# Optimization experiments

Hardware: AMD Instinct MI355X
Metric: run time of the kernel (lower is better)

Reference implementation:

```python
import jax, jax.numpy as jnp
import numpy as np

INPUT_DIM = 1024
HIDDEN_DIM = 1024
NUM_HEADS = 16
HEAD_DIM = HIDDEN_DIM // NUM_HEADS


def setup_inputs() -> dict:
    key = jax.random.key(0)
    ks = jax.random.split(key, 11)
    B, S = 2, 2048
    s_in = 1.0 / np.sqrt(INPUT_DIM)
    s_hid = 1.0 / np.sqrt(HIDDEN_DIM)
    return {
        "query": jax.random.normal(ks[0], (B, S, INPUT_DIM), jnp.float32),
        "key": jax.random.normal(ks[1], (B, S, INPUT_DIM), jnp.float32),
        "value": jax.random.normal(ks[2], (B, S, INPUT_DIM), jnp.float32),
        "Wq": jax.random.normal(ks[3], (INPUT_DIM, HIDDEN_DIM), jnp.float32) * s_in,
        "bq": jnp.zeros((HIDDEN_DIM,), jnp.float32),
        "Wk": jax.random.normal(ks[4], (INPUT_DIM, HEAD_DIM), jnp.float32) * s_in,
        "bk": jnp.zeros((HEAD_DIM,), jnp.float32),
        "Wv": jax.random.normal(ks[5], (INPUT_DIM, HEAD_DIM), jnp.float32) * s_in,
        "bv": jnp.zeros((HEAD_DIM,), jnp.float32),
        "Wo": jax.random.normal(ks[6], (HIDDEN_DIM, INPUT_DIM), jnp.float32) * s_hid,
        "bo": jnp.zeros((INPUT_DIM,), jnp.float32),
    }


def reference(query, key, value, Wq, bq, Wk, bk, Wv, bv, Wo, bo):
    B, S, _ = query.shape
    # projections
    q = query @ Wq + bq                       # [B,S,H*D]
    k = key @ Wk + bk                         # [B,S,D]  (single shared head)
    v = value @ Wv + bv                       # [B,S,D]
    q = q.reshape(B, S, NUM_HEADS, HEAD_DIM)  # [B,S,H,D]
    # MQA scores: shared K broadcast over query heads
    scores = jnp.einsum('bqhd,bkd->bhqk', q, k) / np.sqrt(HIDDEN_DIM)
    attn = jax.nn.softmax(scores, axis=-1)    # [B,H,Q,K]
    out = jnp.einsum('bhqk,bkd->bqhd', attn, v)  # [B,Q,H,D]
    out = out.reshape(B, S, HIDDEN_DIM)
    return out @ Wo + bo
```

## Files before the change

kernel.cpp:

```cpp
#include <hip/hip_runtime.h>


typedef unsigned int   u32;
typedef unsigned short u16;
typedef union { float4 v; float f[4]; } f4u;
typedef __attribute__((ext_vector_type(8)))  short frag16;
typedef __attribute__((ext_vector_type(4)))  float f32x4;
typedef __attribute__((ext_vector_type(16))) float f32x16;
typedef union { frag16 v; u32 w[4]; u16 e[8]; } bf8u;

static __device__ __forceinline__ u16 f2bf(float x) {
  union { float f; u32 u; } v; v.f = x;
  u32 r = v.u + 0x7fff + ((v.u >> 16) & 1);
  return (u16)(r >> 16);
}

static __device__ __forceinline__ u32 cvt_pk_bf16(float lo, float hi) {
  u32 r;
  asm("v_cvt_pk_bf16_f32 %0, %1, %2" : "=v"(r) : "v"(lo), "v"(hi));
  return r;
}

static __device__ __forceinline__ void gload_lds16(const u16* g, u16* l) {
  __builtin_amdgcn_global_load_lds(
      (const __attribute__((address_space(1))) u32*)g,
      (__attribute__((address_space(3))) u32*)l, 16, 0, 0);
}

static __device__ void tcvt_tile(const float* __restrict__ src,
                                 u16* __restrict__ dst,
                                 int C, int ldT, int rt, int ct,
                                 float (*t)[65]) {
  const int r0 = rt * 64, c0 = ct * 64;
  const int tr  = threadIdx.x >> 4;
  const int tc4 = (threadIdx.x & 15) * 4;
#pragma unroll
  for (int i = 0; i < 4; ++i) {
    f4u v; v.v = *(const float4*)(src + (size_t)(r0 + tr + i * 16) * C + c0 + tc4);
    t[tr + i * 16][tc4 + 0] = v.f[0];
    t[tr + i * 16][tc4 + 1] = v.f[1];
    t[tr + i * 16][tc4 + 2] = v.f[2];
    t[tr + i * 16][tc4 + 3] = v.f[3];
  }
  __syncthreads();
#pragma unroll
  for (int i = 0; i < 4; ++i) {
    const int oc = tr + i * 16;
    ushort4 o;
    o.x = f2bf(t[tc4 + 0][oc]);
    o.y = f2bf(t[tc4 + 1][oc]);
    o.z = f2bf(t[tc4 + 2][oc]);
    o.w = f2bf(t[tc4 + 3][oc]);
    *(ushort4*)(dst + (size_t)(c0 + oc) * ldT + r0 + tc4) = o;
  }
}

__global__ __launch_bounds__(256)
void prep_w(const float* __restrict__ Wq, const float* __restrict__ Wo,
            const float* __restrict__ Wk, const float* __restrict__ Wv,
            const float* __restrict__ query,
            u16* __restrict__ wq_t, u16* __restrict__ wo_t,
            u16* __restrict__ wk_t, u16* __restrict__ wv_t,
            u16* __restrict__ xq_bf) {
  const int bid = blockIdx.x;
  if (bid >= 544) {
    const size_t base = (size_t)(bid - 544) * 4096 + threadIdx.x * 16;
    f4u x0, x1, x2, x3;
    x0.v = *(const float4*)(query + base);
    x1.v = *(const float4*)(query + base + 4);
    x2.v = *(const float4*)(query + base + 8);
    x3.v = *(const float4*)(query + base + 12);
    bf8u t0, t1;
    t0.w[0] = cvt_pk_bf16(x0.f[0], x0.f[1]);
    t0.w[1] = cvt_pk_bf16(x0.f[2], x0.f[3]);
    t0.w[2] = cvt_pk_bf16(x1.f[0], x1.f[1]);
    t0.w[3] = cvt_pk_bf16(x1.f[2], x1.f[3]);
    t1.w[0] = cvt_pk_bf16(x2.f[0], x2.f[1]);
    t1.w[1] = cvt_pk_bf16(x2.f[2], x2.f[3]);
    t1.w[2] = cvt_pk_bf16(x3.f[0], x3.f[1]);
    t1.w[3] = cvt_pk_bf16(x3.f[2], x3.f[3]);
    *(frag16*)(xq_bf + base)     = t0.v;
    *(frag16*)(xq_bf + base + 8) = t1.v;
    return;
  }
  __shared__ float t[64][65];
  if (bid < 256)      tcvt_tile(Wq, wq_t, 1024, 1024, bid >> 4, bid & 15, t);
  else if (bid < 512) tcvt_tile(Wo, wo_t, 1024, 1024, (bid - 256) >> 4, (bid - 256) & 15, t);
  else if (bid < 528) tcvt_tile(Wk, wk_t, 64, 1024, bid - 512, 0, t);
  else                tcvt_tile(Wv, wv_t, 64, 1024, bid - 528, 0, t);
}

static __device__ void gemm128n64(const u16* __restrict__ Abf,
                                  const u16* __restrict__ Bt,
                                  const float* __restrict__ bias,
                                  void* __restrict__ Cout, int out_mode,
                                  float oscale, int row0, int col0,
                                  int N, int K, u16* As, u16* Bs) {
  const int tid  = threadIdx.x;
  const int lane = tid & 63;
  const int quad = lane >> 4, l15 = lane & 15;
  const int w = tid >> 6, wy = w >> 1, wx = w & 1;
  const int lrow = lane >> 3, lcol = (lane & 7) * 8;

  f32x4 acc[4][2];
#pragma unroll
  for (int i = 0; i < 4; ++i)
#pragma unroll
    for (int j = 0; j < 2; ++j) {
      acc[i][j][0] = 0.f; acc[i][j][1] = 0.f;
      acc[i][j][2] = 0.f; acc[i][j][3] = 0.f;
    }

  const u16* ag = Abf + (size_t)(row0 + w * 32 + lrow) * K + lcol;
  const u16* bg = Bt  + (size_t)(col0 + w * 16 + lrow) * K + lcol;
  u16* alds = As + w * 4 * 512;
  u16* blds = Bs + w * 2 * 512;

  for (int k0 = 0; k0 < K; k0 += 64) {
    __syncthreads();
#pragma unroll
    for (int i = 0; i < 4; ++i)
      gload_lds16(ag + (size_t)i * 8 * K + k0, alds + i * 512);
#pragma unroll
    for (int i = 0; i < 2; ++i)
      gload_lds16(bg + (size_t)i * 8 * K + k0, blds + i * 512);
    __syncthreads();
#pragma unroll
    for (int ks = 0; ks < 2; ++ks) {
      frag16 af[4], bfr[2];
#pragma unroll
      for (int i = 0; i < 4; ++i)
        af[i] = *(const frag16*)(&As[(wy * 64 + i * 16 + l15) * 64 + ks * 32 + quad * 8]);
#pragma unroll
      for (int j = 0; j < 2; ++j)
        bfr[j] = *(const frag16*)(&Bs[(wx * 32 + j * 16 + l15) * 64 + ks * 32 + quad * 8]);
#pragma unroll
      for (int i = 0; i < 4; ++i)
#pragma unroll
        for (int j = 0; j < 2; ++j)
          acc[i][j] = __builtin_amdgcn_mfma_f32_16x16x32_bf16(af[i], bfr[j], acc[i][j], 0, 0, 0);
    }
  }

  float bj[2];
#pragma unroll
  for (int j = 0; j < 2; ++j)
    bj[j] = bias[col0 + wx * 32 + j * 16 + l15];

#pragma unroll
  for (int i = 0; i < 4; ++i)
#pragma unroll
    for (int rr = 0; rr < 4; ++rr) {
      const size_t row = row0 + wy * 64 + i * 16 + quad * 4 + rr;
#pragma unroll
      for (int j = 0; j < 2; ++j) {
        const float v = (acc[i][j][rr] + bj[j]) * oscale;
        const int col = col0 + wx * 32 + j * 16 + l15;
        if (out_mode == 0) ((float*)Cout)[row * N + col] = v;
        else               ((u16*)Cout)[row * N + col] = f2bf(v);
      }
    }
}

#define GP 72
template <bool A_FP32>
static __device__ void gemm64(const float* __restrict__ Af32,
                              const u16* __restrict__ Abf,
                              const u16* __restrict__ Bt,
                              const float* __restrict__ bias,
                              void* __restrict__ Cout, int out_mode,
                              float oscale,
                              int row0, int col0, int N, int K, int ldT,
                              u16* As, u16* Bs) {
  const int tid  = threadIdx.x;
  const int lane = tid & 63;
  const int quad = lane >> 4, l15 = lane & 15;
  const int w = tid >> 6, wy = w >> 1, wx = w & 1;

  f32x4 acc[2][2];
#pragma unroll
  for (int i = 0; i < 2; ++i)
#pragma unroll
    for (int j = 0; j < 2; ++j) {
      acc[i][j][0] = 0.f; acc[i][j][1] = 0.f;
      acc[i][j][2] = 0.f; acc[i][j][3] = 0.f;
    }

  const int r = tid >> 2, c16 = (tid & 3) * 16;

  for (int k0 = 0; k0 < K; k0 += 64) {
    frag16 a0, a1;
    if (A_FP32) {
      const float* ap = Af32 + (size_t)(row0 + r) * K + k0 + c16;
      f4u x0, x1, x2, x3;
      x0.v = *(const float4*)(ap);
      x1.v = *(const float4*)(ap + 4);
      x2.v = *(const float4*)(ap + 8);
      x3.v = *(const float4*)(ap + 12);
      bf8u t0, t1;
      t0.w[0] = cvt_pk_bf16(x0.f[0], x0.f[1]);
      t0.w[1] = cvt_pk_bf16(x0.f[2], x0.f[3]);
      t0.w[2] = cvt_pk_bf16(x1.f[0], x1.f[1]);
      t0.w[3] = cvt_pk_bf16(x1.f[2], x1.f[3]);
      t1.w[0] = cvt_pk_bf16(x2.f[0], x2.f[1]);
      t1.w[1] = cvt_pk_bf16(x2.f[2], x2.f[3]);
      t1.w[2] = cvt_pk_bf16(x3.f[0], x3.f[1]);
      t1.w[3] = cvt_pk_bf16(x3.f[2], x3.f[3]);
      a0 = t0.v; a1 = t1.v;
    } else {
      const u16* ap = Abf + (size_t)(row0 + r) * K + k0 + c16;
      a0 = *(const frag16*)(ap);
      a1 = *(const frag16*)(ap + 8);
    }
    const u16* bp = Bt + (size_t)(col0 + r) * K + k0 + c16;
    const frag16 b0 = *(const frag16*)(bp);
    const frag16 b1 = *(const frag16*)(bp + 8);
    __syncthreads();
    *(frag16*)(&As[r * GP + c16])     = a0;
    *(frag16*)(&As[r * GP + c16 + 8]) = a1;
    *(frag16*)(&Bs[r * GP + c16])     = b0;
    *(frag16*)(&Bs[r * GP + c16 + 8]) = b1;
    __syncthreads();
#pragma unroll
    for (int ks = 0; ks < 2; ++ks) {
      frag16 af[2], bf[2];
#pragma unroll
      for (int i = 0; i < 2; ++i)
        af[i] = *(const frag16*)(&As[(wy * 32 + i * 16 + l15) * GP + ks * 32 + quad * 8]);
#pragma unroll
      for (int j = 0; j < 2; ++j)
        bf[j] = *(const frag16*)(&Bs[(wx * 32 + j * 16 + l15) * GP + ks * 32 + quad * 8]);
#pragma unroll
      for (int i = 0; i < 2; ++i)
#pragma unroll
        for (int j = 0; j < 2; ++j)
          acc[i][j] = __builtin_amdgcn_mfma_f32_16x16x32_bf16(af[i], bf[j], acc[i][j], 0, 0, 0);
    }
  }

  float bj[2];
#pragma unroll
  for (int j = 0; j < 2; ++j)
    bj[j] = bias[col0 + wx * 32 + j * 16 + l15];

#pragma unroll
  for (int i = 0; i < 2; ++i) {
#pragma unroll
    for (int rr = 0; rr < 4; ++rr) {
      const size_t row = row0 + wy * 32 + i * 16 + quad * 4 + rr;
#pragma unroll
      for (int j = 0; j < 2; ++j) {
        const float v = (acc[i][j][rr] + bj[j]) * oscale;
        const int col = col0 + wx * 32 + j * 16 + l15;
        if (out_mode == 0)      ((float*)Cout)[row * N + col] = v;
        else if (out_mode == 1) ((u16*)Cout)[row * N + col] = f2bf(v);
        else                    ((u16*)Cout)[(size_t)col * ldT + row] = f2bf(v);
      }
    }
  }
}

#define C2_SCALE 0.045084220027780106f

__global__ __launch_bounds__(256, 4)
void proj2(const float* __restrict__ key, const float* __restrict__ value,
           const u16* __restrict__ xq_bf,
           const u16* __restrict__ wq_t, const u16* __restrict__ wk_t,
           const u16* __restrict__ wv_t,
           const float* __restrict__ bq, const float* __restrict__ bk,
           const float* __restrict__ bv,
           u16* __restrict__ q_bf, u16* __restrict__ k_bf,
           u16* __restrict__ vt_bf, int M, int K) {
  __shared__ __align__(16) u16 smem[12288];
  const int bid = blockIdx.x;
  if (bid < 512)
    gemm128n64(xq_bf, wq_t, bq, q_bf, 1, C2_SCALE,
               (bid >> 4) * 128, (bid & 15) * 64, 1024, K, smem, smem + 8192);
  else if (bid < 576)
    gemm64<true>(key, nullptr, wk_t, bk, k_bf, 1, 1.0f,
                 (bid - 512) * 64, 0, 64, K, 0, smem, smem + 64 * GP);
  else
    gemm64<true>(value, nullptr, wv_t, bv, vt_bf, 2, 1.0f,
                 (bid - 576) * 64, 0, 64, K, M, smem, smem + 64 * GP);
}

__global__ __launch_bounds__(256, 4)
void out_proj(const u16* __restrict__ ao, const u16* __restrict__ wo_t,
              const float* __restrict__ bo, float* __restrict__ out,
              int M, int K) {
  __shared__ __align__(16) u16 smem[12288];
  const int bid = blockIdx.x;
  gemm128n64(ao, wo_t, bo, out, 0, 1.0f,
             (bid >> 4) * 128, (bid & 15) * 64, 1024, K, smem, smem + 8192);
}

#define PP 72

__global__ __launch_bounds__(256, 2)
void mqa_flash_mfma(const u16* __restrict__ Qb,
                    const u16* __restrict__ Kb,
                    const u16* __restrict__ Vt,
                    u16* __restrict__ O) {
  const int S = 2048, HID = 1024, D = 64, BS = 4096;
  __shared__ __align__(16) u16 Kss[64 * PP];
  __shared__ __align__(16) u16 Vss[64 * PP];
  __shared__ __align__(16) u16 Ps[4][32 * PP];
  __shared__ float lred[4][32];

  const int tid  = threadIdx.x;
  const int lane = tid & 63;
  const int w    = tid >> 6;
  const int l31  = lane & 31;
  const int hh   = lane >> 5;
  const int qb = blockIdx.x, hg = blockIdx.y, b = blockIdx.z;
  const int h = hg * 4 + w;

  const int sr = tid >> 3;
  const int sc = (tid & 7) * 8;

  const u16* kfb0 = &Kss[l31 * PP + hh * 8];
  const u16* kfb1 = &Kss[(32 + l31) * PP + hh * 8];
  const u16* vfb0 = &Vss[l31 * PP + hh * 8];
  const u16* vfb1 = &Vss[(32 + l31) * PP + hh * 8];
  u16* kw0 = &Kss[sr * PP + sc];
  u16* kw1 = &Kss[(sr + 32) * PP + sc];
  u16* vw0 = &Vss[sr * PP + sc];
  u16* vw1 = &Vss[(sr + 32) * PP + sc];
  u16* psw = Ps[w];
  u16* prow = &psw[l31 * PP];
  const u16* prd = &psw[l31 * PP + hh * 8];

  const u16* qrow = Qb + (size_t)(b * S + qb * 32 + l31) * HID + h * D;
  frag16 qf[4];
#pragma unroll
  for (int ks = 0; ks < 4; ++ks)
    qf[ks] = *(const frag16*)(qrow + ks * 16 + hh * 8);

  f32x16 zero16;
#pragma unroll
  for (int r = 0; r < 16; ++r) zero16[r] = 0.f;
  f32x16 oa0, oa1;
#pragma unroll
  for (int r = 0; r < 16; ++r) { oa0[r] = 0.f; oa1[r] = 0.f; }
  float l_lane = 0.f;

  const u16* kbase = Kb + (size_t)(b * S) * D;
  const u16* vbase = Vt + (size_t)(b * S);

  frag16 pk0 = *(const frag16*)(kbase + (size_t)sr * D + sc);
  frag16 pk1 = *(const frag16*)(kbase + (size_t)(sr + 32) * D + sc);
  frag16 pv0 = *(const frag16*)(vbase + (size_t)sr * BS + sc);
  frag16 pv1 = *(const frag16*)(vbase + (size_t)(sr + 32) * BS + sc);
  *(frag16*)kw0 = pk0;
  *(frag16*)kw1 = pk1;
  *(frag16*)vw0 = pv0;
  *(frag16*)vw1 = pv1;
  pk0 = *(const frag16*)(kbase + (size_t)(64 + sr) * D + sc);
  pk1 = *(const frag16*)(kbase + (size_t)(64 + sr + 32) * D + sc);
  pv0 = *(const frag16*)(vbase + (size_t)sr * BS + 64 + sc);
  pv1 = *(const frag16*)(vbase + (size_t)(sr + 32) * BS + 64 + sc);
  __syncthreads();

  for (int kc = 0; kc < S; kc += 64) {
    frag16 kf0[4], kf1[4], vf0[4], vf1[4];
#pragma unroll
    for (int ks = 0; ks < 4; ++ks) {
      kf0[ks] = *(const frag16*)(kfb0 + ks * 16);
      kf1[ks] = *(const frag16*)(kfb1 + ks * 16);
      vf0[ks] = *(const frag16*)(vfb0 + ks * 16);
      vf1[ks] = *(const frag16*)(vfb1 + ks * 16);
    }
    __syncthreads();

    *(frag16*)kw0 = pk0;
    *(frag16*)kw1 = pk1;
    *(frag16*)vw0 = pv0;
    *(frag16*)vw1 = pv1;

    const int nc = (kc + 128 < S) ? kc + 128 : (S - 64);
    pk0 = *(const frag16*)(kbase + (size_t)(nc + sr) * D + sc);
    pk1 = *(const frag16*)(kbase + (size_t)(nc + sr + 32) * D + sc);
    pv0 = *(const frag16*)(vbase + (size_t)sr * BS + nc + sc);
    pv1 = *(const frag16*)(vbase + (size_t)(sr + 32) * BS + nc + sc);

    f32x16 sa0, sa1;
#pragma unroll
    for (int ks = 0; ks < 4; ++ks)
      sa0 = __builtin_amdgcn_mfma_f32_32x32x16_bf16(kf0[ks], qf[ks], ks ? sa0 : zero16, 0, 0, 0);
#pragma unroll
    for (int ks = 0; ks < 4; ++ks)
      sa1 = __builtin_amdgcn_mfma_f32_32x32x16_bf16(kf1[ks], qf[ks], ks ? sa1 : zero16, 0, 0, 0);

#pragma unroll
    for (int g = 0; g < 4; ++g) {
      const float p0 = __builtin_amdgcn_exp2f(sa0[g * 4 + 0]);
      const float p1 = __builtin_amdgcn_exp2f(sa0[g * 4 + 1]);
      const float p2 = __builtin_amdgcn_exp2f(sa0[g * 4 + 2]);
      const float p3 = __builtin_amdgcn_exp2f(sa0[g * 4 + 3]);
      const float q0 = __builtin_amdgcn_exp2f(sa1[g * 4 + 0]);
      const float q1 = __builtin_amdgcn_exp2f(sa1[g * 4 + 1]);
      const float q2 = __builtin_amdgcn_exp2f(sa1[g * 4 + 2]);
      const float q3 = __builtin_amdgcn_exp2f(sa1[g * 4 + 3]);
      l_lane += ((p0 + p1) + (p2 + p3)) + ((q0 + q1) + (q2 + q3));
      uint2 pk;
      pk.x = cvt_pk_bf16(p0, p1); pk.y = cvt_pk_bf16(p2, p3);
      *(uint2*)(&prow[g * 8 + hh * 4]) = pk;
      uint2 qk;
      qk.x = cvt_pk_bf16(q0, q1); qk.y = cvt_pk_bf16(q2, q3);
      *(uint2*)(&prow[32 + g * 8 + hh * 4]) = qk;
    }

#pragma unroll
    for (int ks = 0; ks < 4; ++ks) {
      const frag16 pf = *(const frag16*)(prd + ks * 16);
      oa0 = __builtin_amdgcn_mfma_f32_32x32x16_bf16(pf, vf0[ks], oa0, 0, 0, 0);
      oa1 = __builtin_amdgcn_mfma_f32_32x32x16_bf16(pf, vf1[ks], oa1, 0, 0, 0);
    }

    __syncthreads();
  }

  l_lane += __shfl_xor(l_lane, 32);
  lred[w][l31] = l_lane;

#pragma unroll
  for (int g2 = 0; g2 < 4; ++g2) {
    const f32x4 lv = *(const f32x4*)(&lred[w][g2 * 8 + hh * 4]);
#pragma unroll
    for (int m = 0; m < 4; ++m) {
      const int r = g2 * 4 + m;
      const int q_local = g2 * 8 + hh * 4 + m;
      const float li = 1.f / lv[m];
      u16* orow = O + (size_t)(b * S + qb * 32 + q_local) * HID + h * D;
      orow[l31]      = f2bf(oa0[r] * li);
      orow[32 + l31] = f2bf(oa1[r] * li);
    }
  }
}

extern "C" void kernel_launch(void* const* d_in, const int* in_sizes, int n_in,
                              void* d_out, int out_size, void* d_ws, size_t ws_size,
                              hipStream_t stream) {
  const float* query = (const float*)d_in[0];
  const float* key   = (const float*)d_in[1];
  const float* value = (const float*)d_in[2];
  const float* Wq    = (const float*)d_in[3];
  const float* bq    = (const float*)d_in[4];
  const float* Wk    = (const float*)d_in[5];
  const float* bk    = (const float*)d_in[6];
  const float* Wv    = (const float*)d_in[7];
  const float* bv    = (const float*)d_in[8];
  const float* Wo    = (const float*)d_in[9];
  const float* bo    = (const float*)d_in[10];
  float* out = (float*)d_out;

  const int B = 2, S = 2048, IN = 1024, HID = 1024, H = 16, D = 64;
  const int M = B * S;
  const size_t MB = 1024 * 1024;

  char* ws = (char*)d_ws;
  u16* q_bf  = (u16*)ws;
  u16* ao_bf = (u16*)(ws + 8 * MB);
  u16* xq_bf = ao_bf;
  u16* k_bf  = (u16*)(ws + 16 * MB);
  u16* vt_bf = (u16*)(ws + 16 * MB + 512 * 1024);
  u16* wq_t  = (u16*)(ws + 17 * MB);
  u16* wo_t  = (u16*)(ws + 19 * MB);
  u16* wk_t  = (u16*)(ws + 21 * MB);
  u16* wv_t  = (u16*)(ws + 21 * MB + 128 * 1024);

  dim3 blk(256);
  prep_w<<<dim3(1568), blk, 0, stream>>>(Wq, Wo, Wk, Wv, query,
                                         wq_t, wo_t, wk_t, wv_t, xq_bf);
  proj2<<<dim3(640), blk, 0, stream>>>(key, value, xq_bf, wq_t, wk_t, wv_t,
                                       bq, bk, bv, q_bf, k_bf, vt_bf, M, IN);
  mqa_flash_mfma<<<dim3(S / 32, H / 4, B), blk, 0, stream>>>(q_bf, k_bf, vt_bf, ao_bf);
  out_proj<<<dim3(512), blk, 0, stream>>>(ao_bf, wo_t, bo, out, M, HID);
}
```

Before: 204.0 us.

## Split MQA attention over two key halves with a separate combine kernel

Splits the flash-attention key loop into two halves processed by separate blocks, writing unnormalized fp32 partial outputs and row sums to workspace. A new combine kernel then adds the partials, normalizes and converts to bf16. The goal is to double the block count for better occupancy across CUs. In exchange it adds an extra launch and substantial fp32 partial traffic (two 16MB buffers), and it only runs when the workspace is large enough. Because the softmax has no max subtraction, the two halves can simply be added.

```diff
diff --git a/kernel.cpp b/kernel.cpp
--- a/kernel.cpp
+++ b/kernel.cpp
@@ -295,26 +295,20 @@
 }
 
 #define PP 72
-
-__global__ __launch_bounds__(256, 2)
-void mqa_flash_mfma(const u16* __restrict__ Qb,
-                    const u16* __restrict__ Kb,
-                    const u16* __restrict__ Vt,
-                    u16* __restrict__ O) {
+#define SPLIT_ROWS 4096
+
+template <int NCHUNK>
+static __device__ void mqa_body(const u16* __restrict__ Qb,
+                                const u16* __restrict__ kbase,
+                                const u16* __restrict__ vbase,
+                                int qb, int h, int b,
+                                f32x16& oa0, f32x16& oa1, float& l_lane,
+                                u16* Kss, u16* Vss, u16* psw) {
   const int S = 2048, HID = 1024, D = 64, BS = 4096;
-  __shared__ __align__(16) u16 Kss[64 * PP];
-  __shared__ __align__(16) u16 Vss[64 * PP];
-  __shared__ __align__(16) u16 Ps[4][32 * PP];
-  __shared__ float lred[4][32];
-
   const int tid  = threadIdx.x;
   const int lane = tid & 63;
-  const int w    = tid >> 6;
   const int l31  = lane & 31;
   const int hh   = lane >> 5;
-  const int qb = blockIdx.x, hg = blockIdx.y, b = blockIdx.z;
-  const int h = hg * 4 + w;
-
   const int sr = tid >> 3;
   const int sc = (tid & 7) * 8;
 
@@ -326,7 +320,6 @@
   u16* kw1 = &Kss[(sr + 32) * PP + sc];
   u16* vw0 = &Vss[sr * PP + sc];
   u16* vw1 = &Vss[(sr + 32) * PP + sc];
-  u16* psw = Ps[w];
   u16* prow = &psw[l31 * PP];
   const u16* prd = &psw[l31 * PP + hh * 8];
 
@@ -339,13 +332,8 @@
   f32x16 zero16;
 #pragma unroll
   for (int r = 0; r < 16; ++r) zero16[r] = 0.f;
-  f32x16 oa0, oa1;
-#pragma unroll
-  for (int r = 0; r < 16; ++r) { oa0[r] = 0.f; oa1[r] = 0.f; }
-  float l_lane = 0.f;
-
-  const u16* kbase = Kb + (size_t)(b * S) * D;
-  const u16* vbase = Vt + (size_t)(b * S);
+
+  const int KEYS = NCHUNK * 64;
 
   frag16 pk0 = *(const frag16*)(kbase + (size_t)sr * D + sc);
   frag16 pk1 = *(const frag16*)(kbase + (size_t)(sr + 32) * D + sc);
@@ -361,7 +349,7 @@
   pv1 = *(const frag16*)(vbase + (size_t)(sr + 32) * BS + 64 + sc);
   __syncthreads();
 
-  for (int kc = 0; kc < S; kc += 64) {
+  for (int kc = 0; kc < KEYS; kc += 64) {
     frag16 kf0[4], kf1[4], vf0[4], vf1[4];
 #pragma unroll
     for (int ks = 0; ks < 4; ++ks) {
@@ -377,7 +365,7 @@
     *(frag16*)vw0 = pv0;
     *(frag16*)vw1 = pv1;
 
-    const int nc = (kc + 128 < S) ? kc + 128 : (S - 64);
+    const int nc = (kc + 128 < KEYS) ? kc + 128 : (KEYS - 64);
     pk0 = *(const frag16*)(kbase + (size_t)(nc + sr) * D + sc);
     pk1 = *(const frag16*)(kbase + (size_t)(nc + sr + 32) * D + sc);
     pv0 = *(const frag16*)(vbase + (size_t)sr * BS + nc + sc);
@@ -419,6 +407,104 @@
 
     __syncthreads();
   }
+}
+
+__global__ __launch_bounds__(256, 4)
+void mqa_flash_split(const u16* __restrict__ Qb, const u16* __restrict__ Kb,
+                     const u16* __restrict__ Vt,
+                     float* __restrict__ Opart,
+                     float* __restrict__ Lpart) {
+  const int S = 2048, HID = 1024, D = 64;
+  __shared__ __align__(16) u16 Kss[64 * PP];
+  __shared__ __align__(16) u16 Vss[64 * PP];
+  __shared__ __align__(16) u16 Ps[4][32 * PP];
+  __shared__ float lred[4][32];
+
+  const int tid  = threadIdx.x;
+  const int lane = tid & 63;
+  const int w    = tid >> 6;
+  const int l31  = lane & 31;
+  const int hh   = lane >> 5;
+  const int qb = blockIdx.x, hg = blockIdx.y;
+  const int b  = blockIdx.z >> 1, h2 = blockIdx.z & 1;
+  const int h = hg * 4 + w;
+
+  f32x16 oa0, oa1;
+#pragma unroll
+  for (int r = 0; r < 16; ++r) { oa0[r] = 0.f; oa1[r] = 0.f; }
+  float l_lane = 0.f;
+
+  const u16* kbase = Kb + (size_t)(b * S + h2 * 1024) * D;
+  const u16* vbase = Vt + (size_t)(b * S) + h2 * 1024;
+
+  mqa_body<16>(Qb, kbase, vbase, qb, h, b, oa0, oa1, l_lane, Kss, Vss, Ps[w]);
+
+  l_lane += __shfl_xor(l_lane, 32);
+  const int brow = b * S + qb * 32;
+  if (lane < 32)
+    Lpart[((size_t)h2 * SPLIT_ROWS + brow + l31) * 16 + h] = l_lane;
+
+  float* obase = Opart + (size_t)h2 * SPLIT_ROWS * 1024;
+#pragma unroll
+  for (int g2 = 0; g2 < 4; ++g2) {
+#pragma unroll
+    for (int m = 0; m < 4; ++m) {
+      const int r = g2 * 4 + m;
+      const int q_local = g2 * 8 + hh * 4 + m;
+      float* orow = obase + (size_t)(brow + q_local) * HID + h * D;
+      orow[l31]      = oa0[r];
+      orow[32 + l31] = oa1[r];
+    }
+  }
+}
+
+__global__ __launch_bounds__(256)
+void mqa_combine(const float* __restrict__ Opart, const float* __restrict__ Lpart,
+                 u16* __restrict__ ao) {
+  const int row = blockIdx.x;
+  const int tid = threadIdx.x;
+  const size_t base = (size_t)row * 1024 + tid * 4;
+  f4u a, c;
+  a.v = *(const float4*)(Opart + base);
+  c.v = *(const float4*)(Opart + (size_t)SPLIT_ROWS * 1024 + base);
+  const int hidx = tid >> 4;
+  const float l0 = Lpart[(size_t)row * 16 + hidx];
+  const float l1 = Lpart[((size_t)SPLIT_ROWS + row) * 16 + hidx];
+  const float li = 1.f / (l0 + l1);
+  ushort4 o;
+  o.x = f2bf((a.f[0] + c.f[0]) * li);
+  o.y = f2bf((a.f[1] + c.f[1]) * li);
+  o.z = f2bf((a.f[2] + c.f[2]) * li);
+  o.w = f2bf((a.f[3] + c.f[3]) * li);
+  *(ushort4*)(ao + base) = o;
+}
+
+__global__ __launch_bounds__(256, 2)
+void mqa_flash_mfma(const u16* __restrict__ Qb, const u16* __restrict__ Kb,
+                    const u16* __restrict__ Vt, u16* __restrict__ O) {
+  const int S = 2048, HID = 1024, D = 64;
+  __shared__ __align__(16) u16 Kss[64 * PP];
+  __shared__ __align__(16) u16 Vss[64 * PP];
+  __shared__ __align__(16) u16 Ps[4][32 * PP];
+  __shared__ float lred[4][32];
+
+  const int tid  = threadIdx.x;
+  const int lane = tid & 63;
+  const int w    = tid >> 6;
+  const int l31  = lane & 31;
+  const int hh   = lane >> 5;
+  const int qb = blockIdx.x, hg = blockIdx.y, b = blockIdx.z;
+  const int h = hg * 4 + w;
+
+  f32x16 oa0, oa1;
+#pragma unroll
+  for (int r = 0; r < 16; ++r) { oa0[r] = 0.f; oa1[r] = 0.f; }
+  float l_lane = 0.f;
+
+  const u16* kbase = Kb + (size_t)(b * S) * D;
+  const u16* vbase = Vt + (size_t)(b * S);
+
+  mqa_body<32>(Qb, kbase, vbase, qb, h, b, oa0, oa1, l_lane, Kss, Vss, Ps[w]);
 
   l_lane += __shfl_xor(l_lane, 32);
   lred[w][l31] = l_lane;
@@ -468,12 +554,21 @@
   u16* wo_t  = (u16*)(ws + 19 * MB);
   u16* wk_t  = (u16*)(ws + 21 * MB);
   u16* wv_t  = (u16*)(ws + 21 * MB + 128 * 1024);
+  float* opart = (float*)(ws + 22 * MB);
+  float* lpart = (float*)(ws + 54 * MB);
+  const bool can_split = ws_size >= (size_t)55 * MB;
 
   dim3 blk(256);
   prep_w<<<dim3(1568), blk, 0, stream>>>(Wq, Wo, Wk, Wv, query,
                                          wq_t, wo_t, wk_t, wv_t, xq_bf);
   proj2<<<dim3(640), blk, 0, stream>>>(key, value, xq_bf, wq_t, wk_t, wv_t,
                                        bq, bk, bv, q_bf, k_bf, vt_bf, M, IN);
-  mqa_flash_mfma<<<dim3(S / 32, H / 4, B), blk, 0, stream>>>(q_bf, k_bf, vt_bf, ao_bf);
+  if (can_split) {
+    mqa_flash_split<<<dim3(S / 32, H / 4, B * 2), blk, 0, stream>>>(
+        q_bf, k_bf, vt_bf, opart, lpart);
+    mqa_combine<<<dim3(M), blk, 0, stream>>>(opart, lpart, ao_bf);
+  } else {
+    mqa_flash_mfma<<<dim3(S / 32, H / 4, B), blk, 0, stream>>>(q_bf, k_bf, vt_bf, ao_bf);
+  }
   out_proj<<<dim3(512), blk, 0, stream>>>(ao_bf, wo_t, bo, out, M, HID);
 }
```

Result: slower. 237.7 us (+16.5%).
